# Kernel optimization log

Measured on AMD Instinct MI355X. Metric: run time of the kernel, lower is better.

## Reference

```python
import jax, jax.numpy as jnp
import numpy as np

H_DIM, N_HEAD, FF_DIM, B_GRAPHS, MAX_N = 256, 8, 1024, 16, 512
LENGTHS = np.array([512, 480, 448, 416, 384, 352, 320, 288] * 2)  # ragged graph sizes, sum = 6400
N_NODES = int(LENGTHS.sum())
N_EDGES = 16 * N_NODES  # avg degree 16


def setup_inputs() -> dict:
    key = jax.random.key(0)
    kq, kk, kv, ko, k1, k2, kh = jax.random.split(key, 7)
    offsets = np.concatenate([[0], np.cumsum(LENGTHS)[:-1]])
    batch_np = np.repeat(np.arange(B_GRAPHS), LENGTHS)
    rng = np.random.default_rng(0)
    src = rng.integers(0, N_NODES, N_EDGES)
    g = batch_np[src]
    dst = offsets[g] + rng.integers(0, LENGTHS[g])  # dst in same graph as src
    edge_index = jnp.asarray(np.stack([src, dst]), dtype=jnp.int32)
    batch = jnp.asarray(batch_np, dtype=jnp.int32)

    def w(k, shape):
        return 0.02 * jax.random.normal(k, shape, dtype=jnp.float32)

    return dict(
        h=jax.random.normal(kh, (N_NODES, H_DIM), dtype=jnp.float32),
        Wq=w(kq, (H_DIM, H_DIM)), bq=jnp.zeros(H_DIM),
        Wk=w(kk, (H_DIM, H_DIM)), bk=jnp.zeros(H_DIM),
        Wv=w(kv, (H_DIM, H_DIM)), bv=jnp.zeros(H_DIM),
        Wo=w(ko, (H_DIM, H_DIM)), bo=jnp.zeros(H_DIM),
        W1=w(k1, (FF_DIM, H_DIM)), b1=jnp.zeros(FF_DIM),
        W2=w(k2, (H_DIM, FF_DIM)), b2=jnp.zeros(H_DIM),
        g1=jnp.ones(H_DIM), be1=jnp.zeros(H_DIM),
        g2=jnp.ones(H_DIM), be2=jnp.zeros(H_DIM),
        batch=batch, edge_index=edge_index,
        num_graphs=B_GRAPHS, max_n=MAX_N, n_head=N_HEAD,
    )


def _layernorm(x, g, b, eps=1e-5):
    mu = x.mean(-1, keepdims=True)
    var = ((x - mu) ** 2).mean(-1, keepdims=True)
    return (x - mu) * jax.lax.rsqrt(var + eps) * g + b


def reference(h, Wq, bq, Wk, bk, Wv, bv, Wo, bo, W1, b1, W2, b2, g1, be1, g2, be2,
              batch, edge_index, num_graphs, max_n, n_head):
    N, H = h.shape
    dh = H // n_head
    # position of each node inside its graph (batch is sorted by graph)
    counts = jax.ops.segment_sum(jnp.ones(N, jnp.int32), batch, num_segments=num_graphs)
    offsets = jnp.concatenate([jnp.zeros(1, jnp.int32), jnp.cumsum(counts)[:-1].astype(jnp.int32)])
    pos = jnp.arange(N, dtype=jnp.int32) - offsets[batch]
    # to_dense_batch: pad ragged nodes into [B, S, H]
    x = jnp.zeros((num_graphs, max_n, H), h.dtype).at[batch, pos].set(h)
    # to_dense_adj + _canonical_mask: faithful to source, EDGES get -inf (True -> -inf)
    src, dst = edge_index[0], edge_index[1]
    adj = jnp.zeros((num_graphs, max_n, max_n), bool).at[batch[src], pos[src], pos[dst]].set(True)
    attn_mask = jnp.where(adj, -jnp.inf, 0.0)[:, None, :, :]  # [B,1,S,S], broadcast over heads

    def proj(W, b):
        return (x @ W.T + b).reshape(num_graphs, max_n, n_head, dh).transpose(0, 2, 1, 3)

    q = proj(Wq, bq)
    k = proj(Wk, bk)
    v = proj(Wk, bk)  # faithful to source: V_x uses self.K
    scores = jax.nn.softmax(attn_mask + jnp.einsum('bhsd,bhtd->bhst', q, k) / np.sqrt(dh).astype(h.dtype), axis=-1)
    att = jnp.einsum('bhst,bhtd->bhsd', scores, v).transpose(0, 2, 1, 3).reshape(num_graphs, max_n, H)
    att = att @ Wo.T + bo
    h_att = att[batch, pos]  # from_dense_batch: unpad back to [N, H]
    h1 = _layernorm(h_att + h, g1, be1)
    ff = jax.nn.relu(h1 @ W1.T + b1) @ W2.T + b2
    return _layernorm(ff + h1, g2, be2)
```

## Files before the change

kernel.cpp:

```cpp
#include <hip/hip_runtime.h>
#include <math.h>

typedef unsigned int u32;
typedef unsigned short ushort_t;
typedef __attribute__((ext_vector_type(8))) short short8;
typedef __attribute__((ext_vector_type(4))) float f32x4;
typedef __attribute__((ext_vector_type(16))) float f32x16;

#define B_G 16
#define S_MAX 512
#define NH 8
#define DH 32
#define HD 256
#define FFD 1024
#define ADJW 16

__device__ __forceinline__ ushort_t f2bf(float f) {
  u32 u = __float_as_uint(f);
  u += 0x7fffu + ((u >> 16) & 1u);
  return (ushort_t)(u >> 16);
}

__device__ __forceinline__ void gll16(const void* g, void* l) {
  __builtin_amdgcn_global_load_lds(
      (const __attribute__((address_space(1))) unsigned int*)g,
      (__attribute__((address_space(3))) unsigned int*)l, 16, 0, 0);
}

__global__ __launch_bounds__(256) void k_prep(u32* __restrict__ adj,
    const int* __restrict__ batch, int N, int* __restrict__ offs,
    const float* __restrict__ bq, const float* __restrict__ bk,
    float* __restrict__ bqk) {
  int tid = threadIdx.x, blk = blockIdx.x;
  uint4 z = {0u, 0u, 0u, 0u};
  ((uint4*)adj)[blk * 256 + tid] = z;
  if (blk == 0) {
    bqk[tid] = bq[tid];
    bqk[HD + tid] = bk[tid];
    if (tid <= B_G) {
      if (tid == B_G) { offs[B_G] = N; }
      else {
        int lo = 0, hi = N;
        while (lo < hi) { int mid = (lo + hi) >> 1; if (batch[mid] < tid) lo = mid + 1; else hi = mid; }
        offs[tid] = lo;
      }
    }
  }
}

__global__ __launch_bounds__(256) void k_mega(
    const float* __restrict__ h, const int* __restrict__ offs, ushort_t* __restrict__ xb,
    const int* __restrict__ ei, int E, const int* __restrict__ batch, u32* __restrict__ adj,
    const float* __restrict__ wa, const float* __restrict__ wb, const float* __restrict__ wc,
    const float* __restrict__ wd, const float* __restrict__ we,
    ushort_t* __restrict__ oa, ushort_t* __restrict__ ob, ushort_t* __restrict__ oc,
    ushort_t* __restrict__ od, ushort_t* __restrict__ oe) {
  int blk = blockIdx.x, tid = threadIdx.x;
  if (blk < 2048) {
    int row = blk * 4 + (tid >> 6);
    int c = tid & 63;
    int b = row >> 9, pos = row & 511;
    int len = offs[b + 1] - offs[b];
    uint2 pk = {0u, 0u};
    if (pos < len) {
      int node = offs[b] + pos;
      float4 v = ((const float4*)(h + (size_t)node * HD))[c];
      pk.x = (u32)f2bf(v.x) | ((u32)f2bf(v.y) << 16);
      pk.y = (u32)f2bf(v.z) | ((u32)f2bf(v.w) << 16);
    }
    *(uint2*)(xb + (size_t)row * HD + c * 4) = pk;
  } else if (blk < 2448) {
    int e = (blk - 2048) * 256 + tid;
    if (e >= E) return;
    int s = ei[e], d = ei[E + e];
    int b = batch[s];
    int o = offs[b];
    atomicOr(&adj[(b * S_MAX + (s - o)) * ADJW + ((d - o) >> 5)], 1u << ((d - o) & 31));
  } else {
    int bb = blk - 2448;
    const float* src; ushort_t* dst; int off;
    if (bb < 32)       { src = wa; dst = oa; off = bb; }
    else if (bb < 64)  { src = wb; dst = ob; off = bb - 32; }
    else if (bb < 96)  { src = wc; dst = oc; off = bb - 64; }
    else if (bb < 224) { src = wd; dst = od; off = bb - 96; }
    else               { src = we; dst = oe; off = bb - 224; }
    size_t i = (size_t)off * 2048 + tid * 8;
    float4 v0 = *(const float4*)&src[i];
    float4 v1 = *(const float4*)&src[i + 4];
    uint4 pk;
    pk.x = (u32)f2bf(v0.x) | ((u32)f2bf(v0.y) << 16);
    pk.y = (u32)f2bf(v0.z) | ((u32)f2bf(v0.w) << 16);
    pk.z = (u32)f2bf(v1.x) | ((u32)f2bf(v1.y) << 16);
    pk.w = (u32)f2bf(v1.z) | ((u32)f2bf(v1.w) << 16);
    *(uint4*)&dst[i] = pk;
  }
}

template<bool RELU, bool OUTBF>
__global__ __launch_bounds__(512) void k_mgemm(const ushort_t* __restrict__ A,
    const ushort_t* __restrict__ W, const float* __restrict__ bias,
    void* __restrict__ Cout, int Ncols, int Kdim) {
  __shared__ __align__(16) ushort_t As[2][128 * 64];
  __shared__ __align__(16) ushort_t Bs[2][128 * 64];
  int tid = threadIdx.x;
  int wid = tid >> 6, lane = tid & 63;
  int wm = wid >> 2, wn = wid & 3;
  int arow0 = blockIdx.x * 128, bcol0 = blockIdx.y * 128;

  const ushort_t* gA[2]; const ushort_t* gB[2];
  int dofs[2];
  #pragma unroll
  for (int i = 0; i < 2; i++) {
    int s = i * 512 + tid;
    int r = s >> 3, ck = (s & 7) ^ (r & 7);
    gA[i] = A + (size_t)(arow0 + r) * Kdim + ck * 8;
    gB[i] = W + (size_t)(bcol0 + r) * Kdim + ck * 8;
    dofs[i] = (i * 512 + wid * 64) * 8;
  }

  f32x4 acc[4][2];
  #pragma unroll
  for (int i = 0; i < 4; i++)
    #pragma unroll
    for (int j = 0; j < 2; j++) { f32x4 z = {0.f,0.f,0.f,0.f}; acc[i][j] = z; }

  #pragma unroll
  for (int i = 0; i < 2; i++) { gll16(gA[i], &As[0][dofs[i]]); gll16(gB[i], &Bs[0][dofs[i]]); }
  asm volatile("s_waitcnt vmcnt(0)" ::: "memory");
  __builtin_amdgcn_s_barrier();

  int nsteps = Kdim >> 6;
  int cur = 0;
  for (int ks = 0; ks < nsteps; ks++) {
    if (ks + 1 < nsteps) {
      int k0n = (ks + 1) << 6;
      #pragma unroll
      for (int i = 0; i < 2; i++) {
        gll16(gA[i] + k0n, &As[cur ^ 1][dofs[i]]);
        gll16(gB[i] + k0n, &Bs[cur ^ 1][dofs[i]]);
      }
    }
    #pragma unroll
    for (int kk = 0; kk < 2; kk++) {
      short8 af[4], bfv[2];
      #pragma unroll
      for (int i = 0; i < 4; i++) {
        int row = wm * 64 + i * 16 + (lane & 15);
        int ck = (kk * 4 + (lane >> 4)) ^ (row & 7);
        af[i] = *(const short8*)&As[cur][row * 64 + ck * 8];
      }
      #pragma unroll
      for (int j = 0; j < 2; j++) {
        int row = wn * 32 + j * 16 + (lane & 15);
        int ck = (kk * 4 + (lane >> 4)) ^ (row & 7);
        bfv[j] = *(const short8*)&Bs[cur][row * 64 + ck * 8];
      }
      #pragma unroll
      for (int i = 0; i < 4; i++)
        #pragma unroll
        for (int j = 0; j < 2; j++)
          acc[i][j] = __builtin_amdgcn_mfma_f32_16x16x32_bf16(af[i], bfv[j], acc[i][j], 0, 0, 0);
    }
    asm volatile("s_waitcnt vmcnt(0)" ::: "memory");
    __builtin_amdgcn_s_barrier();
    cur ^= 1;
  }

  float bj[2]; int colb[2];
  #pragma unroll
  for (int j = 0; j < 2; j++) {
    colb[j] = bcol0 + wn * 32 + j * 16 + (lane & 15);
    bj[j] = bias[colb[j]];
  }
  #pragma unroll
  for (int i = 0; i < 4; i++) {
    #pragma unroll
    for (int r = 0; r < 4; r++) {
      int row = arow0 + wm * 64 + i * 16 + (lane >> 4) * 4 + r;
      #pragma unroll
      for (int j = 0; j < 2; j++) {
        float v = acc[i][j][r] + bj[j];
        if (RELU) v = fmaxf(v, 0.f);
        if (OUTBF) ((ushort_t*)Cout)[(size_t)row * Ncols + colb[j]] = f2bf(v);
        else       ((float*)Cout)[(size_t)row * Ncols + colb[j]] = v;
      }
    }
  }
}

template<bool OUTBF>
__global__ __launch_bounds__(256) void k_gemm_ln(const ushort_t* __restrict__ A,
    const ushort_t* __restrict__ W, const float* __restrict__ bias,
    const float* __restrict__ R, const float* __restrict__ gamma,
    const float* __restrict__ beta, float* __restrict__ outF,
    ushort_t* __restrict__ outB, int Kdim) {
  __shared__ __align__(16) ushort_t As[2][32 * 64];
  __shared__ __align__(16) ushort_t Bs[2][256 * 64];
  __shared__ float red_s[32 * 4];
  __shared__ float red_q[32 * 4];
  int tid = threadIdx.x;
  int wid = tid >> 6, lane = tid & 63;
  int wn = wid;
  int row0 = blockIdx.x * 32;

  const ushort_t* gA; int dofsA;
  {
    int r = tid >> 3, ck = (tid & 7) ^ (r & 7);
    gA = A + (size_t)(row0 + r) * Kdim + ck * 8;
    dofsA = (wid * 64) * 8;
  }
  const ushort_t* gB[8]; int dofsB[8];
  #pragma unroll
  for (int i = 0; i < 8; i++) {
    int s = i * 256 + tid;
    int r = s >> 3, ck = (s & 7) ^ (r & 7);
    gB[i] = W + (size_t)r * Kdim + ck * 8;
    dofsB[i] = (i * 256 + wid * 64) * 8;
  }

  f32x4 acc[2][4];
  #pragma unroll
  for (int i = 0; i < 2; i++)
    #pragma unroll
    for (int n = 0; n < 4; n++) { f32x4 z = {0.f,0.f,0.f,0.f}; acc[i][n] = z; }

  gll16(gA, &As[0][dofsA]);
  #pragma unroll
  for (int i = 0; i < 8; i++) gll16(gB[i], &Bs[0][dofsB[i]]);
  asm volatile("s_waitcnt vmcnt(0)" ::: "memory");
  __builtin_amdgcn_s_barrier();

  int nsteps = Kdim >> 6;
  int cur = 0;
  for (int ks = 0; ks < nsteps; ks++) {
    if (ks + 1 < nsteps) {
      int k0n = (ks + 1) << 6;
      gll16(gA + k0n, &As[cur ^ 1][dofsA]);
      #pragma unroll
      for (int i = 0; i < 8; i++) gll16(gB[i] + k0n, &Bs[cur ^ 1][dofsB[i]]);
    }
    #pragma unroll
    for (int kk = 0; kk < 2; kk++) {
      short8 af[2], bfv[4];
      #pragma unroll
      for (int i = 0; i < 2; i++) {
        int row = i * 16 + (lane & 15);
        int ck = (kk * 4 + (lane >> 4)) ^ (row & 7);
        af[i] = *(const short8*)&As[cur][row * 64 + ck * 8];
      }
      #pragma unroll
      for (int n = 0; n < 4; n++) {
        int row = wn * 64 + n * 16 + (lane & 15);
        int ck = (kk * 4 + (lane >> 4)) ^ (row & 7);
        bfv[n] = *(const short8*)&Bs[cur][row * 64 + ck * 8];
      }
      #pragma unroll
      for (int i = 0; i < 2; i++)
        #pragma unroll
        for (int n = 0; n < 4; n++)
          acc[i][n] = __builtin_amdgcn_mfma_f32_16x16x32_bf16(af[i], bfv[n], acc[i][n], 0, 0, 0);
    }
    asm volatile("s_waitcnt vmcnt(0)" ::: "memory");
    __builtin_amdgcn_s_barrier();
    cur ^= 1;
  }

  int col[4]; float bc[4], gm[4], bt[4];
  #pragma unroll
  for (int n = 0; n < 4; n++) {
    col[n] = wn * 64 + n * 16 + (lane & 15);
    bc[n] = bias[col[n]]; gm[n] = gamma[col[n]]; bt[n] = beta[col[n]];
  }
  #pragma unroll
  for (int i = 0; i < 2; i++) {
    #pragma unroll
    for (int r = 0; r < 4; r++) {
      int row_l = i * 16 + (lane >> 4) * 4 + r;
      const float* Rrow = R + (size_t)(row0 + row_l) * HD;
      float s = 0.f, q = 0.f;
      #pragma unroll
      for (int n = 0; n < 4; n++) {
        float v = acc[i][n][r] + bc[n] + Rrow[col[n]];
        acc[i][n][r] = v;
        s += v; q += v * v;
      }
      #pragma unroll
      for (int o = 1; o < 16; o <<= 1) { s += __shfl_xor(s, o, 64); q += __shfl_xor(q, o, 64); }
      if ((lane & 15) == 0) { red_s[row_l * 4 + wn] = s; red_q[row_l * 4 + wn] = q; }
    }
  }
  __syncthreads();
  #pragma unroll
  for (int i = 0; i < 2; i++) {
    #pragma unroll
    for (int r = 0; r < 4; r++) {
      int row_l = i * 16 + (lane >> 4) * 4 + r;
      float ssum = red_s[row_l * 4] + red_s[row_l * 4 + 1] + red_s[row_l * 4 + 2] + red_s[row_l * 4 + 3];
      float qsum = red_q[row_l * 4] + red_q[row_l * 4 + 1] + red_q[row_l * 4 + 2] + red_q[row_l * 4 + 3];
      float mu = ssum * (1.f / HD);
      float var = qsum * (1.f / HD) - mu * mu;
      float inv = rsqrtf(var + 1e-5f);
      size_t rb = (size_t)(row0 + row_l) * HD;
      #pragma unroll
      for (int n = 0; n < 4; n++) {
        float v = (acc[i][n][r] - mu) * inv * gm[n] + bt[n];
        outF[rb + col[n]] = v;
        if (OUTBF) outB[rb + col[n]] = f2bf(v);
      }
    }
  }
}

__global__ __launch_bounds__(256) void k_attn(const ushort_t* __restrict__ qkb,
    const u32* __restrict__ adj, const int* __restrict__ offs,
    ushort_t* __restrict__ attOb) {
  int bid = blockIdx.x;
  int qtr = bid & 3, hh = (bid >> 2) & 7, b = bid >> 5;
  int nstart = offs[b], len = offs[b + 1] - nstart;
  int q0blk = qtr * 128;
  if (q0blk >= len) return;

  __shared__ __align__(16) ushort_t K_lds[4 * 512 * 8];
  __shared__ __align__(16) ushort_t Kt_lds[64 * 32 * 8];
  __shared__ __align__(16) ushort_t P_lds[4 * 4 * 32 * 8];

  int tid = threadIdx.x;
  {
    const ushort_t* kg = qkb + (size_t)(b * S_MAX) * 512 + 256 + hh * 32;
    for (int t = tid; t < 512; t += 256) {
      const uint4* src = (const uint4*)(kg + (size_t)t * 512);
      uint4 v0 = src[0], v1 = src[1], v2 = src[2], v3 = src[3];
      *(uint4*)&K_lds[0 * 4096 + t * 8] = v0;
      *(uint4*)&K_lds[1 * 4096 + t * 8] = v1;
      *(uint4*)&K_lds[2 * 4096 + t * 8] = v2;
      *(uint4*)&K_lds[3 * 4096 + t * 8] = v3;
    }
  }
  __syncthreads();
  {
    int d = tid & 31, tg = tid >> 5;
    int cc = d >> 3, e = d & 7;
    for (int i = 0; i < 8; i++) {
      int t0 = tg * 64 + i * 8;
      u32 w0 = (u32)K_lds[cc * 4096 + (t0 + 0) * 8 + e] | ((u32)K_lds[cc * 4096 + (t0 + 1) * 8 + e] << 16);
      u32 w1 = (u32)K_lds[cc * 4096 + (t0 + 2) * 8 + e] | ((u32)K_lds[cc * 4096 + (t0 + 3) * 8 + e] << 16);
      u32 w2 = (u32)K_lds[cc * 4096 + (t0 + 4) * 8 + e] | ((u32)K_lds[cc * 4096 + (t0 + 5) * 8 + e] << 16);
      u32 w3 = (u32)K_lds[cc * 4096 + (t0 + 6) * 8 + e] | ((u32)K_lds[cc * 4096 + (t0 + 7) * 8 + e] << 16);
      uint4 pk = {w0, w1, w2, w3};
      *(uint4*)&Kt_lds[(t0 >> 3) * 256 + d * 8] = pk;
    }
  }
  __syncthreads();

  int w = tid >> 6, lane = tid & 63;
  int q0w = q0blk + w * 32;
  if (q0w >= len) return;

  int lq = lane & 31, hf = lane >> 5;
  int q_abs = q0w + lq;
  const float SCALE = 0.17677669529663687f;

  size_t qrow = (size_t)(b * S_MAX + q_abs) * 512 + hh * 32;
  short8 qf0 = *(const short8*)(qkb + qrow + hf * 8);
  short8 qf1 = *(const short8*)(qkb + qrow + 16 + hf * 8);

  const uint4* ap = (const uint4*)(adj + (size_t)(b * S_MAX + q_abs) * ADJW);
  uint4 a0 = ap[0], a1 = ap[1], a2 = ap[2], a3 = ap[3];
  u32 aw[16] = {a0.x, a0.y, a0.z, a0.w, a1.x, a1.y, a1.z, a1.w,
                a2.x, a2.y, a2.z, a2.w, a3.x, a3.y, a3.z, a3.w};

  f32x16 oacc = {0.f,0.f,0.f,0.f,0.f,0.f,0.f,0.f,0.f,0.f,0.f,0.f,0.f,0.f,0.f,0.f};
  float lsum = 0.f;

  #pragma unroll
  for (int tt = 0; tt < 16; tt++) {
    int t0 = tt * 32;
    short8 ka0 = *(const short8*)&K_lds[hf * 4096 + (t0 + lq) * 8];
    short8 ka1 = *(const short8*)&K_lds[(2 + hf) * 4096 + (t0 + lq) * 8];
    f32x16 sc = {0.f,0.f,0.f,0.f,0.f,0.f,0.f,0.f,0.f,0.f,0.f,0.f,0.f,0.f,0.f,0.f};
    sc = __builtin_amdgcn_mfma_f32_32x32x16_bf16(ka0, qf0, sc, 0, 0, 0);
    sc = __builtin_amdgcn_mfma_f32_32x32x16_bf16(ka1, qf1, sc, 0, 0, 0);
    u32 word = aw[tt];
    float p[16];
    #pragma unroll
    for (int r = 0; r < 16; r++) {
      int tb = (r & 3) + 8 * (r >> 2) + 4 * hf;
      float pe = __expf(sc[r] * SCALE);
      p[r] = ((word >> tb) & 1u) ? 0.f : pe;
      lsum += p[r];
    }
    #pragma unroll
    for (int g = 0; g < 4; g++) {
      u32 lo = (u32)f2bf(p[4 * g]) | ((u32)f2bf(p[4 * g + 1]) << 16);
      u32 hi = (u32)f2bf(p[4 * g + 2]) | ((u32)f2bf(p[4 * g + 3]) << 16);
      uint2 pk = {lo, hi};
      *(uint2*)&P_lds[w * 1024 + g * 256 + lq * 8 + hf * 4] = pk;
    }
    short8 va0 = *(const short8*)&Kt_lds[(t0 / 8 + hf) * 256 + lq * 8];
    short8 va1 = *(const short8*)&Kt_lds[(t0 / 8 + 2 + hf) * 256 + lq * 8];
    short8 pb0 = *(const short8*)&P_lds[w * 1024 + hf * 256 + lq * 8];
    short8 pb1 = *(const short8*)&P_lds[w * 1024 + (2 + hf) * 256 + lq * 8];
    oacc = __builtin_amdgcn_mfma_f32_32x32x16_bf16(va0, pb0, oacc, 0, 0, 0);
    oacc = __builtin_amdgcn_mfma_f32_32x32x16_bf16(va1, pb1, oacc, 0, 0, 0);
  }

  float ltot = lsum + __shfl_xor(lsum, 32, 64);
  float inv = 1.f / ltot;
  if (q_abs < len) {
    int node = nstart + q_abs;
    ushort_t* op = attOb + (size_t)node * HD + hh * DH;
    #pragma unroll
    for (int g = 0; g < 4; g++) {
      float v0 = oacc[4 * g] * inv, v1 = oacc[4 * g + 1] * inv;
      float v2 = oacc[4 * g + 2] * inv, v3 = oacc[4 * g + 3] * inv;
      u32 lo = (u32)f2bf(v0) | ((u32)f2bf(v1) << 16);
      u32 hi = (u32)f2bf(v2) | ((u32)f2bf(v3) << 16);
      uint2 pk = {lo, hi};
      *(uint2*)(op + g * 8 + hf * 4) = pk;
    }
  }
}

extern "C" void kernel_launch(void* const* d_in, const int* in_sizes, int n_in,
                              void* d_out, int out_size, void* d_ws, size_t ws_size,
                              hipStream_t stream) {
  const float* h   = (const float*)d_in[0];
  const float* Wq  = (const float*)d_in[1];
  const float* bq  = (const float*)d_in[2];
  const float* Wk  = (const float*)d_in[3];
  const float* bk  = (const float*)d_in[4];
  const float* Wo  = (const float*)d_in[7];
  const float* bo  = (const float*)d_in[8];
  const float* W1  = (const float*)d_in[9];
  const float* b1  = (const float*)d_in[10];
  const float* W2  = (const float*)d_in[11];
  const float* b2  = (const float*)d_in[12];
  const float* g1  = (const float*)d_in[13];
  const float* be1 = (const float*)d_in[14];
  const float* g2  = (const float*)d_in[15];
  const float* be2 = (const float*)d_in[16];
  const int* batch = (const int*)d_in[17];
  const int* ei    = (const int*)d_in[18];
  int N = in_sizes[0] / HD;
  int E = in_sizes[18] / 2;

  char* ws = (char*)d_ws;
  ushort_t* xb    = (ushort_t*)(ws);
  ushort_t* attOb = xb;
  ushort_t* qkb   = (ushort_t*)(ws + ((size_t)4 << 20));
  float*    h1    = (float*)(ws + ((size_t)12 << 20));
  ushort_t* h1b   = (ushort_t*)(ws + ((size_t)19 << 20));
  ushort_t* ff1b  = (ushort_t*)(ws + ((size_t)23 << 20));
  char* wbase = ws + ((size_t)36 << 20);
  ushort_t* Wqkb = (ushort_t*)(wbase);
  ushort_t* Wob  = (ushort_t*)(wbase + (256 << 10));
  ushort_t* W1b  = (ushort_t*)(wbase + (384 << 10));
  ushort_t* W2b  = (ushort_t*)(wbase + (896 << 10));
  float*    bqk  = (float*)(wbase + (1408 << 10));
  u32*      adj  = (u32*)(wbase + (1536 << 10));
  int*      offs = (int*)(ws + ((size_t)38 << 20));

  k_prep<<<128, 256, 0, stream>>>(adj, batch, N, offs, bq, bk, bqk);
  k_mega<<<2800, 256, 0, stream>>>(h, offs, xb, ei, E, batch, adj,
                                   Wq, Wk, Wo, W1, W2,
                                   Wqkb, Wqkb + 65536, Wob, W1b, W2b);
  k_mgemm<false, true><<<dim3(64, 4), 512, 0, stream>>>(xb, Wqkb, bqk, qkb, 512, HD);
  k_attn<<<B_G * NH * 4, 256, 0, stream>>>(qkb, adj, offs, attOb);
  k_gemm_ln<true><<<200, 256, 0, stream>>>(attOb, Wob, bo, h, g1, be1, h1, h1b, HD);
  k_mgemm<true, true><<<dim3(50, 8), 512, 0, stream>>>(h1b, W1b, b1, ff1b, FFD, HD);
  k_gemm_ln<false><<<200, 256, 0, stream>>>(ff1b, W2b, b2, h1, g2, be2, (float*)d_out, nullptr, FFD);
}
```

Baseline: 90.65 us.

## Skip padded rows in QK projection and attention, fold padded-key contribution analytically

The QK projection now runs on the unpadded node array, so rows beyond each graph's length are no longer built or multiplied, and the dense padded copy of the activations goes away. The attention loop now covers only the real key tiles. The padded keys, whose key and value both reduce to the key bias, are added back in closed form: `exp(q·bk·scale)` times the pad count goes into the softmax denominator, and that weight times `bk` goes into the output. Edge scattering moves into the QK GEMM kernel and the prep work merges into a single kernel, which removes one launch. The GEMM tile shrinks to 64x128 with 256 threads to give more blocks. The code assumes graph lengths are multiples of 32: a partial tail tile would silently drop keys, and query rows past a graph's end would be written into the next graph's rows.

```diff
diff --git a/kernel.cpp b/kernel.cpp
--- a/kernel.cpp
+++ b/kernel.cpp
@@ -20,6 +20,9 @@
   u += 0x7fffu + ((u >> 16) & 1u);
   return (ushort_t)(u >> 16);
 }
+__device__ __forceinline__ float bf2f(ushort_t s) {
+  return __uint_as_float(((u32)s) << 16);
+}
 
 __device__ __forceinline__ void gll16(const void* g, void* l) {
   __builtin_amdgcn_global_load_lds(
@@ -27,14 +30,19 @@
       (__attribute__((address_space(3))) unsigned int*)l, 16, 0, 0);
 }
 
-__global__ __launch_bounds__(256) void k_prep(u32* __restrict__ adj,
+__global__ __launch_bounds__(256) void k_prep2(u32* __restrict__ adj,
     const int* __restrict__ batch, int N, int* __restrict__ offs,
-    const float* __restrict__ bq, const float* __restrict__ bk,
-    float* __restrict__ bqk) {
-  int tid = threadIdx.x, blk = blockIdx.x;
-  uint4 z = {0u, 0u, 0u, 0u};
-  ((uint4*)adj)[blk * 256 + tid] = z;
-  if (blk == 0) {
+    const float* __restrict__ bq, const float* __restrict__ bk, float* __restrict__ bqk,
+    const float* __restrict__ wa, const float* __restrict__ wb, const float* __restrict__ wc,
+    const float* __restrict__ wd, const float* __restrict__ we,
+    ushort_t* __restrict__ oa, ushort_t* __restrict__ ob, ushort_t* __restrict__ oc,
+    ushort_t* __restrict__ od, ushort_t* __restrict__ oe,
+    const float* __restrict__ h, ushort_t* __restrict__ hb) {
+  int blk = blockIdx.x, tid = threadIdx.x;
+  if (blk < 128) {
+    uint4 z = {0u, 0u, 0u, 0u};
+    ((uint4*)adj)[blk * 256 + tid] = z;
+  } else if (blk == 128) {
     bqk[tid] = bq[tid];
     bqk[HD + tid] = bk[tid];
     if (tid <= B_G) {
@@ -45,39 +53,8 @@
         offs[tid] = lo;
       }
     }
-  }
-}
-
-__global__ __launch_bounds__(256) void k_mega(
-    const float* __restrict__ h, const int* __restrict__ offs, ushort_t* __restrict__ xb,
-    const int* __restrict__ ei, int E, const int* __restrict__ batch, u32* __restrict__ adj,
-    const float* __restrict__ wa, const float* __restrict__ wb, const float* __restrict__ wc,
-    const float* __restrict__ wd, const float* __restrict__ we,
-    ushort_t* __restrict__ oa, ushort_t* __restrict__ ob, ushort_t* __restrict__ oc,
-    ushort_t* __restrict__ od, ushort_t* __restrict__ oe) {
-  int blk = blockIdx.x, tid = threadIdx.x;
-  if (blk < 2048) {
-    int row = blk * 4 + (tid >> 6);
-    int c = tid & 63;
-    int b = row >> 9, pos = row & 511;
-    int len = offs[b + 1] - offs[b];
-    uint2 pk = {0u, 0u};
-    if (pos < len) {
-      int node = offs[b] + pos;
-      float4 v = ((const float4*)(h + (size_t)node * HD))[c];
-      pk.x = (u32)f2bf(v.x) | ((u32)f2bf(v.y) << 16);
-      pk.y = (u32)f2bf(v.z) | ((u32)f2bf(v.w) << 16);
-    }
-    *(uint2*)(xb + (size_t)row * HD + c * 4) = pk;
-  } else if (blk < 2448) {
-    int e = (blk - 2048) * 256 + tid;
-    if (e >= E) return;
-    int s = ei[e], d = ei[E + e];
-    int b = batch[s];
-    int o = offs[b];
-    atomicOr(&adj[(b * S_MAX + (s - o)) * ADJW + ((d - o) >> 5)], 1u << ((d - o) & 31));
-  } else {
-    int bb = blk - 2448;
+  } else if (blk < 481) {
+    int bb = blk - 129;
     const float* src; ushort_t* dst; int off;
     if (bb < 32)       { src = wa; dst = oa; off = bb; }
     else if (bb < 64)  { src = wb; dst = ob; off = bb - 32; }
@@ -93,39 +70,69 @@
     pk.z = (u32)f2bf(v1.x) | ((u32)f2bf(v1.y) << 16);
     pk.w = (u32)f2bf(v1.z) | ((u32)f2bf(v1.w) << 16);
     *(uint4*)&dst[i] = pk;
-  }
-}
-
-template<bool RELU, bool OUTBF>
-__global__ __launch_bounds__(512) void k_mgemm(const ushort_t* __restrict__ A,
+  } else {
+    size_t i = ((size_t)(blk - 481) * 256 + tid) * 8;
+    float4 v0 = *(const float4*)&h[i];
+    float4 v1 = *(const float4*)&h[i + 4];
+    uint4 pk;
+    pk.x = (u32)f2bf(v0.x) | ((u32)f2bf(v0.y) << 16);
+    pk.y = (u32)f2bf(v0.z) | ((u32)f2bf(v0.w) << 16);
+    pk.z = (u32)f2bf(v1.x) | ((u32)f2bf(v1.y) << 16);
+    pk.w = (u32)f2bf(v1.z) | ((u32)f2bf(v1.w) << 16);
+    *(uint4*)&hb[i] = pk;
+  }
+}
+
+template<bool RELU, bool DOEDGE>
+__global__ __launch_bounds__(256) void k_mgemm(const ushort_t* __restrict__ A,
     const ushort_t* __restrict__ W, const float* __restrict__ bias,
-    void* __restrict__ Cout, int Ncols, int Kdim) {
-  __shared__ __align__(16) ushort_t As[2][128 * 64];
+    ushort_t* __restrict__ Cout, int Ncols, int Kdim, int gridx,
+    const int* __restrict__ ei, int E, const int* __restrict__ batch,
+    const int* __restrict__ offs, u32* __restrict__ adj) {
+  __shared__ __align__(16) ushort_t As[2][64 * 64];
   __shared__ __align__(16) ushort_t Bs[2][128 * 64];
   int tid = threadIdx.x;
   int wid = tid >> 6, lane = tid & 63;
-  int wm = wid >> 2, wn = wid & 3;
-  int arow0 = blockIdx.x * 128, bcol0 = blockIdx.y * 128;
-
-  const ushort_t* gA[2]; const ushort_t* gB[2];
-  int dofs[2];
+  int wm = wid & 1, wn = wid >> 1;
+  int arow0 = blockIdx.x * 64, bcol0 = blockIdx.y * 128;
+
+  if (DOEDGE) {
+    int e = (blockIdx.y * gridx + blockIdx.x) * 256 + tid;
+    if (e < E) {
+      int s = ei[e], d = ei[E + e];
+      int b = batch[s];
+      int o = offs[b];
+      atomicOr(&adj[(b * S_MAX + (s - o)) * ADJW + ((d - o) >> 5)], 1u << ((d - o) & 31));
+    }
+  }
+
+  const ushort_t* gA[2]; const ushort_t* gB[4];
+  int dofsA[2], dofsB[4];
   #pragma unroll
   for (int i = 0; i < 2; i++) {
-    int s = i * 512 + tid;
+    int s = i * 256 + wid * 64 + lane;
     int r = s >> 3, ck = (s & 7) ^ (r & 7);
     gA[i] = A + (size_t)(arow0 + r) * Kdim + ck * 8;
+    dofsA[i] = (i * 256 + wid * 64) * 8;
+  }
+  #pragma unroll
+  for (int i = 0; i < 4; i++) {
+    int s = i * 256 + wid * 64 + lane;
+    int r = s >> 3, ck = (s & 7) ^ (r & 7);
     gB[i] = W + (size_t)(bcol0 + r) * Kdim + ck * 8;
-    dofs[i] = (i * 512 + wid * 64) * 8;
-  }
-
-  f32x4 acc[4][2];
-  #pragma unroll
-  for (int i = 0; i < 4; i++)
-    #pragma unroll
-    for (int j = 0; j < 2; j++) { f32x4 z = {0.f,0.f,0.f,0.f}; acc[i][j] = z; }
-
-  #pragma unroll
-  for (int i = 0; i < 2; i++) { gll16(gA[i], &As[0][dofs[i]]); gll16(gB[i], &Bs[0][dofs[i]]); }
+    dofsB[i] = (i * 256 + wid * 64) * 8;
+  }
+
+  f32x4 acc[2][4];
+  #pragma unroll
+  for (int i = 0; i < 2; i++)
+    #pragma unroll
+    for (int j = 0; j < 4; j++) { f32x4 z = {0.f,0.f,0.f,0.f}; acc[i][j] = z; }
+
+  #pragma unroll
+  for (int i = 0; i < 2; i++) gll16(gA[i], &As[0][dofsA[i]]);
+  #pragma unroll
+  for (int i = 0; i < 4; i++) gll16(gB[i], &Bs[0][dofsB[i]]);
   asm volatile("s_waitcnt vmcnt(0)" ::: "memory");
   __builtin_amdgcn_s_barrier();
 
@@ -135,30 +142,29 @@
     if (ks + 1 < nsteps) {
       int k0n = (ks + 1) << 6;
       #pragma unroll
+      for (int i = 0; i < 2; i++) gll16(gA[i] + k0n, &As[cur ^ 1][dofsA[i]]);
+      #pragma unroll
+      for (int i = 0; i < 4; i++) gll16(gB[i] + k0n, &Bs[cur ^ 1][dofsB[i]]);
+    }
+    #pragma unroll
+    for (int kk = 0; kk < 2; kk++) {
+      short8 af[2], bfv[4];
+      #pragma unroll
       for (int i = 0; i < 2; i++) {
-        gll16(gA[i] + k0n, &As[cur ^ 1][dofs[i]]);
-        gll16(gB[i] + k0n, &Bs[cur ^ 1][dofs[i]]);
-      }
-    }
-    #pragma unroll
-    for (int kk = 0; kk < 2; kk++) {
-      short8 af[4], bfv[2];
-      #pragma unroll
-      for (int i = 0; i < 4; i++) {
-        int row = wm * 64 + i * 16 + (lane & 15);
+        int row = wm * 32 + i * 16 + (lane & 15);
         int ck = (kk * 4 + (lane >> 4)) ^ (row & 7);
         af[i] = *(const short8*)&As[cur][row * 64 + ck * 8];
       }
       #pragma unroll
-      for (int j = 0; j < 2; j++) {
-        int row = wn * 32 + j * 16 + (lane & 15);
+      for (int j = 0; j < 4; j++) {
+        int row = wn * 64 + j * 16 + (lane & 15);
         int ck = (kk * 4 + (lane >> 4)) ^ (row & 7);
         bfv[j] = *(const short8*)&Bs[cur][row * 64 + ck * 8];
       }
       #pragma unroll
-      for (int i = 0; i < 4; i++)
+      for (int i = 0; i < 2; i++)
         #pragma unroll
-        for (int j = 0; j < 2; j++)
+        for (int j = 0; j < 4; j++)
           acc[i][j] = __builtin_amdgcn_mfma_f32_16x16x32_bf16(af[i], bfv[j], acc[i][j], 0, 0, 0);
     }
     asm volatile("s_waitcnt vmcnt(0)" ::: "memory");
@@ -166,23 +172,22 @@
     cur ^= 1;
   }
 
-  float bj[2]; int colb[2];
-  #pragma unroll
-  for (int j = 0; j < 2; j++) {
-    colb[j] = bcol0 + wn * 32 + j * 16 + (lane & 15);
+  float bj[4]; int colb[4];
+  #pragma unroll
+  for (int j = 0; j < 4; j++) {
+    colb[j] = bcol0 + wn * 64 + j * 16 + (lane & 15);
     bj[j] = bias[colb[j]];
   }
   #pragma unroll
-  for (int i = 0; i < 4; i++) {
+  for (int i = 0; i < 2; i++) {
     #pragma unroll
     for (int r = 0; r < 4; r++) {
-      int row = arow0 + wm * 64 + i * 16 + (lane >> 4) * 4 + r;
-      #pragma unroll
-      for (int j = 0; j < 2; j++) {
+      int row = arow0 + wm * 32 + i * 16 + (lane >> 4) * 4 + r;
+      #pragma unroll
+      for (int j = 0; j < 4; j++) {
         float v = acc[i][j][r] + bj[j];
         if (RELU) v = fmaxf(v, 0.f);
-        if (OUTBF) ((ushort_t*)Cout)[(size_t)row * Ncols + colb[j]] = f2bf(v);
-        else       ((float*)Cout)[(size_t)row * Ncols + colb[j]] = v;
+        Cout[(size_t)row * Ncols + colb[j]] = f2bf(v);
       }
     }
   }
@@ -313,12 +318,13 @@
 
 __global__ __launch_bounds__(256) void k_attn(const ushort_t* __restrict__ qkb,
     const u32* __restrict__ adj, const int* __restrict__ offs,
-    ushort_t* __restrict__ attOb) {
+    const float* __restrict__ bqk, ushort_t* __restrict__ attOb) {
   int bid = blockIdx.x;
   int qtr = bid & 3, hh = (bid >> 2) & 7, b = bid >> 5;
   int nstart = offs[b], len = offs[b + 1] - nstart;
   int q0blk = qtr * 128;
   if (q0blk >= len) return;
+  int lenT = len >> 5;
 
   __shared__ __align__(16) ushort_t K_lds[4 * 512 * 8];
   __shared__ __align__(16) ushort_t Kt_lds[64 * 32 * 8];
@@ -326,8 +332,8 @@
 
   int tid = threadIdx.x;
   {
-    const ushort_t* kg = qkb + (size_t)(b * S_MAX) * 512 + 256 + hh * 32;
-    for (int t = tid; t < 512; t += 256) {
+    const ushort_t* kg = qkb + (size_t)nstart * 512 + 256 + hh * 32;
+    for (int t = tid; t < len; t += 256) {
       const uint4* src = (const uint4*)(kg + (size_t)t * 512);
       uint4 v0 = src[0], v1 = src[1], v2 = src[2], v3 = src[3];
       *(uint4*)&K_lds[0 * 4096 + t * 8] = v0;
@@ -342,12 +348,14 @@
     int cc = d >> 3, e = d & 7;
     for (int i = 0; i < 8; i++) {
       int t0 = tg * 64 + i * 8;
-      u32 w0 = (u32)K_lds[cc * 4096 + (t0 + 0) * 8 + e] | ((u32)K_lds[cc * 4096 + (t0 + 1) * 8 + e] << 16);
-      u32 w1 = (u32)K_lds[cc * 4096 + (t0 + 2) * 8 + e] | ((u32)K_lds[cc * 4096 + (t0 + 3) * 8 + e] << 16);
-      u32 w2 = (u32)K_lds[cc * 4096 + (t0 + 4) * 8 + e] | ((u32)K_lds[cc * 4096 + (t0 + 5) * 8 + e] << 16);
-      u32 w3 = (u32)K_lds[cc * 4096 + (t0 + 6) * 8 + e] | ((u32)K_lds[cc * 4096 + (t0 + 7) * 8 + e] << 16);
-      uint4 pk = {w0, w1, w2, w3};
-      *(uint4*)&Kt_lds[(t0 >> 3) * 256 + d * 8] = pk;
+      if (t0 < len) {
+        u32 w0 = (u32)K_lds[cc * 4096 + (t0 + 0) * 8 + e] | ((u32)K_lds[cc * 4096 + (t0 + 1) * 8 + e] << 16);
+        u32 w1 = (u32)K_lds[cc * 4096 + (t0 + 2) * 8 + e] | ((u32)K_lds[cc * 4096 + (t0 + 3) * 8 + e] << 16);
+        u32 w2 = (u32)K_lds[cc * 4096 + (t0 + 4) * 8 + e] | ((u32)K_lds[cc * 4096 + (t0 + 5) * 8 + e] << 16);
+        u32 w3 = (u32)K_lds[cc * 4096 + (t0 + 6) * 8 + e] | ((u32)K_lds[cc * 4096 + (t0 + 7) * 8 + e] << 16);
+        uint4 pk = {w0, w1, w2, w3};
+        *(uint4*)&Kt_lds[(t0 >> 3) * 256 + d * 8] = pk;
+      }
     }
   }
   __syncthreads();
@@ -357,14 +365,13 @@
   if (q0w >= len) return;
 
   int lq = lane & 31, hf = lane >> 5;
-  int q_abs = q0w + lq;
   const float SCALE = 0.17677669529663687f;
 
-  size_t qrow = (size_t)(b * S_MAX + q_abs) * 512 + hh * 32;
+  size_t qrow = (size_t)(nstart + q0w + lq) * 512 + hh * 32;
   short8 qf0 = *(const short8*)(qkb + qrow + hf * 8);
   short8 qf1 = *(const short8*)(qkb + qrow + 16 + hf * 8);
 
-  const uint4* ap = (const uint4*)(adj + (size_t)(b * S_MAX + q_abs) * ADJW);
+  const uint4* ap = (const uint4*)(adj + (size_t)(b * S_MAX + q0w + lq) * ADJW);
   uint4 a0 = ap[0], a1 = ap[1], a2 = ap[2], a3 = ap[3];
   u32 aw[16] = {a0.x, a0.y, a0.z, a0.w, a1.x, a1.y, a1.z, a1.w,
                 a2.x, a2.y, a2.z, a2.w, a3.x, a3.y, a3.z, a3.w};
@@ -372,8 +379,7 @@
   f32x16 oacc = {0.f,0.f,0.f,0.f,0.f,0.f,0.f,0.f,0.f,0.f,0.f,0.f,0.f,0.f,0.f,0.f};
   float lsum = 0.f;
 
-  #pragma unroll
-  for (int tt = 0; tt < 16; tt++) {
+  for (int tt = 0; tt < lenT; tt++) {
     int t0 = tt * 32;
     short8 ka0 = *(const short8*)&K_lds[hf * 4096 + (t0 + lq) * 8];
     short8 ka1 = *(const short8*)&K_lds[(2 + hf) * 4096 + (t0 + lq) * 8];
@@ -404,15 +410,26 @@
     oacc = __builtin_amdgcn_mfma_f32_32x32x16_bf16(va1, pb1, oacc, 0, 0, 0);
   }
 
-  float ltot = lsum + __shfl_xor(lsum, 32, 64);
+  const float* bkh = bqk + 256 + hh * 32;
+  float pq = 0.f;
+  #pragma unroll
+  for (int j = 0; j < 8; j++) pq += bf2f((ushort_t)qf0[j]) * bkh[hf * 8 + j];
+  #pragma unroll
+  for (int j = 0; j < 8; j++) pq += bf2f((ushort_t)qf1[j]) * bkh[16 + hf * 8 + j];
+  pq += __shfl_xor(pq, 32, 64);
+  float pe_pad = __expf(pq * SCALE) * (float)(S_MAX - len);
+
+  float ltot = lsum + __shfl_xor(lsum, 32, 64) + pe_pad;
   float inv = 1.f / ltot;
-  if (q_abs < len) {
-    int node = nstart + q_abs;
+  {
+    int node = nstart + q0w + lq;
     ushort_t* op = attOb + (size_t)node * HD + hh * DH;
     #pragma unroll
     for (int g = 0; g < 4; g++) {
-      float v0 = oacc[4 * g] * inv, v1 = oacc[4 * g + 1] * inv;
-      float v2 = oacc[4 * g + 2] * inv, v3 = oacc[4 * g + 3] * inv;
+      float v0 = (oacc[4 * g]     + pe_pad * bkh[g * 8 + hf * 4 + 0]) * inv;
+      float v1 = (oacc[4 * g + 1] + pe_pad * bkh[g * 8 + hf * 4 + 1]) * inv;
+      float v2 = (oacc[4 * g + 2] + pe_pad * bkh[g * 8 + hf * 4 + 2]) * inv;
+      float v3 = (oacc[4 * g + 3] + pe_pad * bkh[g * 8 + hf * 4 + 3]) * inv;
       u32 lo = (u32)f2bf(v0) | ((u32)f2bf(v1) << 16);
       u32 hi = (u32)f2bf(v2) | ((u32)f2bf(v3) << 16);
       uint2 pk = {lo, hi};
@@ -445,8 +462,8 @@
   int E = in_sizes[18] / 2;
 
   char* ws = (char*)d_ws;
-  ushort_t* xb    = (ushort_t*)(ws);
-  ushort_t* attOb = xb;
+  ushort_t* hb    = (ushort_t*)(ws);
+  ushort_t* attOb = hb;
   ushort_t* qkb   = (ushort_t*)(ws + ((size_t)4 << 20));
   float*    h1    = (float*)(ws + ((size_t)12 << 20));
   ushort_t* h1b   = (ushort_t*)(ws + ((size_t)19 << 20));
@@ -460,13 +477,14 @@
   u32*      adj  = (u32*)(wbase + (1536 << 10));
   int*      offs = (int*)(ws + ((size_t)38 << 20));
 
-  k_prep<<<128, 256, 0, stream>>>(adj, batch, N, offs, bq, bk, bqk);
-  k_mega<<<2800, 256, 0, stream>>>(h, offs, xb, ei, E, batch, adj,
-                                   Wq, Wk, Wo, W1, W2,
-                                   Wqkb, Wqkb + 65536, Wob, W1b, W2b);
-  k_mgemm<false, true><<<dim3(64, 4), 512, 0, stream>>>(xb, Wqkb, bqk, qkb, 512, HD);
-  k_attn<<<B_G * NH * 4, 256, 0, stream>>>(qkb, adj, offs, attOb);
+  k_prep2<<<1281, 256, 0, stream>>>(adj, batch, N, offs, bq, bk, bqk,
+                                    Wq, Wk, Wo, W1, W2,
+                                    Wqkb, Wqkb + 65536, Wob, W1b, W2b, h, hb);
+  k_mgemm<false, true><<<dim3(100, 4), 256, 0, stream>>>(hb, Wqkb, bqk, qkb, 512, HD, 100,
+                                                         ei, E, batch, offs, adj);
+  k_attn<<<B_G * NH * 4, 256, 0, stream>>>(qkb, adj, offs, bqk, attOb);
   k_gemm_ln<true><<<200, 256, 0, stream>>>(attOb, Wob, bo, h, g1, be1, h1, h1b, HD);
-  k_mgemm<true, true><<<dim3(50, 8), 512, 0, stream>>>(h1b, W1b, b1, ff1b, FFD, HD);
+  k_mgemm<true, false><<<dim3(100, 8), 256, 0, stream>>>(h1b, W1b, b1, ff1b, FFD, HD, 100,
+                                                         nullptr, 0, nullptr, nullptr, nullptr);
   k_gemm_ln<false><<<200, 256, 0, stream>>>(ff1b, W2b, b2, h1, g2, be2, (float*)d_out, nullptr, FFD);
 }
```

Result: faster. 88.07 us (-2.8%).
